# Kernel tuning notes

Measured on AMD Instinct MI355X. Metric: run time of the kernel, lower is better.

The kernel has to match this reference:

```python
import jax, jax.numpy as jnp
import numpy as np

N = 100000
E = 3200000
F_IN = 128
HID = 64
NUM_GRAPHS = 512
NUM_CLASSES = 2


def setup_inputs() -> dict:
    key = jax.random.key(0)
    ks = jax.random.split(key, 8)
    x = jax.random.normal(ks[0], (N, F_IN), dtype=jnp.float32)
    edge_index = jax.random.randint(ks[1], (2, E), 0, N, dtype=jnp.int64)
    batch = jnp.sort(jax.random.randint(ks[2], (N,), 0, NUM_GRAPHS, dtype=jnp.int64))
    # Glorot-style init for GCN weights, PyTorch default-style for fc
    W1 = jax.random.normal(ks[3], (F_IN, HID), dtype=jnp.float32) * (1.0 / np.sqrt(F_IN))
    b1 = jnp.zeros((HID,), dtype=jnp.float32)
    W2 = jax.random.normal(ks[4], (HID, HID), dtype=jnp.float32) * (1.0 / np.sqrt(HID))
    b2 = jnp.zeros((HID,), dtype=jnp.float32)
    Wfc = jax.random.normal(ks[5], (HID, NUM_CLASSES), dtype=jnp.float32) * (1.0 / np.sqrt(HID))
    bfc = jax.random.normal(ks[6], (NUM_CLASSES,), dtype=jnp.float32) * 0.01
    return {"x": x, "edge_index": edge_index, "batch": batch,
            "W1": W1, "b1": b1, "W2": W2, "b2": b2, "Wfc": Wfc, "bfc": bfc}


def _gcn_conv(x, row, col, deg_inv_sqrt, W, b):
    """PyG GCNConv: out[col] += d^{-1/2}[row] d^{-1/2}[col] * (x W)[row], self-loops included in row/col."""
    h = x @ W  # [N, out_dim]
    norm = deg_inv_sqrt[row] * deg_inv_sqrt[col]  # [E+N]
    msgs = h[row] * norm[:, None]  # gather + scale
    out = jax.ops.segment_sum(msgs, col, num_segments=N)  # scatter-add
    return out + b


def reference(x, edge_index, batch, W1, b1, W2, b2, Wfc, bfc):
    # add self-loops once (shared normalization for both layers)
    loop = jnp.arange(N, dtype=edge_index.dtype)
    row = jnp.concatenate([edge_index[0], loop])  # sources
    col = jnp.concatenate([edge_index[1], loop])  # targets
    deg = jax.ops.segment_sum(jnp.ones_like(col, dtype=x.dtype), col, num_segments=N)
    deg_inv_sqrt = jnp.where(deg > 0, jax.lax.rsqrt(deg), 0.0)

    h = jax.nn.relu(_gcn_conv(x, row, col, deg_inv_sqrt, W1, b1))
    h = jax.nn.relu(_gcn_conv(h, row, col, deg_inv_sqrt, W2, b2))

    # global_mean_pool over batch ids
    sums = jax.ops.segment_sum(h, batch, num_segments=NUM_GRAPHS)  # [G, HID]
    counts = jax.ops.segment_sum(jnp.ones((N,), dtype=h.dtype), batch, num_segments=NUM_GRAPHS)
    pooled = sums / jnp.maximum(counts, 1.0)[:, None]

    # dropout p=0.5 is identity in eval mode
    return pooled @ Wfc + bfc  # [G, NUM_CLASSES]
```

## Files before the change

kernel.cpp:

```cpp
#include <hip/hip_runtime.h>

#define N_NODES   100000
#define N_EDGES   3200000
#define F_INP     128
#define HID       64
#define N_GRAPHS  512
#define N_CLASSES 2
#define NB        782
#define SCAT_BLOCKS 1024
#define CHUNK     (N_EDGES / SCAT_BLOCKS)

__device__ __forceinline__ unsigned short f2bf(float f) {
    unsigned int u = __float_as_uint(f);
    return (unsigned short)((u + 0x7FFFu + ((u >> 16) & 1u)) >> 16);
}
__device__ __forceinline__ float bf_lo(unsigned int u) { return __uint_as_float(u << 16); }
__device__ __forceinline__ float bf_hi(unsigned int u) { return __uint_as_float(u & 0xFFFF0000u); }

__global__ __launch_bounds__(256) void hist_kernel(const int* __restrict__ ei,
                                                   int* __restrict__ bcnt,
                                                   int* __restrict__ bh) {
    __shared__ int hist[NB];
    for (int i = threadIdx.x; i < NB; i += 256) hist[i] = 0;
    __syncthreads();
    const int e0 = blockIdx.x * CHUNK, e1 = e0 + CHUNK;
    for (int e = e0 + threadIdx.x; e < e1; e += 256)
        atomicAdd(&hist[ei[N_EDGES + e] >> 7], 1);
    __syncthreads();
    for (int i = threadIdx.x; i < NB; i += 256) {
        int v = hist[i];
        bh[(size_t)blockIdx.x * NB + i] = v;
        if (v) atomicAdd(&bcnt[i], v);
    }
}

__global__ __launch_bounds__(1024) void scan_kernel(const int* __restrict__ bcnt,
                                                    int* __restrict__ boff) {
    __shared__ int s[1024];
    const int tid = threadIdx.x;
    const int v = (tid < NB) ? bcnt[tid] : 0;
    s[tid] = v;
    __syncthreads();
    for (int d = 1; d < 1024; d <<= 1) {
        int t = (tid >= d) ? s[tid - d] : 0;
        __syncthreads();
        s[tid] += t;
        __syncthreads();
    }
    if (tid <= NB) boff[tid] = s[tid] - v;
}

__global__ __launch_bounds__(64) void bbase_kernel(int* __restrict__ bh,
                                                   const int* __restrict__ boff) {
    const int b = blockIdx.x * 64 + threadIdx.x;
    if (b >= NB) return;
    int base = boff[b];
    for (int i = 0; i < SCAT_BLOCKS; i += 8) {
        int v[8];
#pragma unroll
        for (int j = 0; j < 8; ++j) v[j] = bh[(size_t)(i + j) * NB + b];
#pragma unroll
        for (int j = 0; j < 8; ++j) { bh[(size_t)(i + j) * NB + b] = base; base += v[j]; }
    }
}

__global__ __launch_bounds__(256) void scatter_kernel(const int* __restrict__ ei,
                                                      const int* __restrict__ bh,
                                                      int* __restrict__ pairs) {
    __shared__ int lbase[NB];
    __shared__ int lcur[NB];
    for (int i = threadIdx.x; i < NB; i += 256) {
        lbase[i] = bh[(size_t)blockIdx.x * NB + i];
        lcur[i] = 0;
    }
    __syncthreads();
    const int e0 = blockIdx.x * CHUNK, e1 = e0 + CHUNK;
    for (int e = e0 + threadIdx.x; e < e1; e += 256) {
        int c = ei[N_EDGES + e];
        int r = ei[e];
        int b = c >> 7;
        int off = atomicAdd(&lcur[b], 1);
        pairs[lbase[b] + off] = r | ((c & 127) << 17);
    }
}

__global__ __launch_bounds__(256) void csr_kernel(const int* __restrict__ pairs,
                                                  const int* __restrict__ boff,
                                                  int* __restrict__ adj,
                                                  int* __restrict__ offs,
                                                  float* __restrict__ dis) {
    __shared__ int cnt[128];
    __shared__ int sc[128];
    __shared__ int base[128];
    __shared__ int cur[128];
    const int tid = threadIdx.x;
    const int b = blockIdx.x;
    const int beg = boff[b], end = boff[b + 1];
    if (tid < 128) { cnt[tid] = 0; cur[tid] = 0; }
    __syncthreads();
    for (int e = beg + tid; e < end; e += 256)
        atomicAdd(&cnt[pairs[e] >> 17], 1);
    __syncthreads();
    if (tid < 128) sc[tid] = cnt[tid];
    __syncthreads();
    for (int d = 1; d < 128; d <<= 1) {
        int t = (tid >= d && tid < 128) ? sc[tid - d] : 0;
        __syncthreads();
        if (tid < 128) sc[tid] += t;
        __syncthreads();
    }
    if (tid < 128) base[tid] = beg + sc[tid] - cnt[tid];
    __syncthreads();
    for (int e = beg + tid; e < end; e += 256) {
        int v = pairs[e];
        int lc = v >> 17;
        int o = atomicAdd(&cur[lc], 1);
        adj[base[lc] + o] = v & 131071;
    }
    const int n = (b << 7) + tid;
    if (tid < 128 && n < N_NODES) {
        offs[n] = base[tid];
        dis[n] = rsqrtf((float)cnt[tid] + 1.0f);
    }
    if (b == 0 && tid == 0) offs[N_NODES] = N_EDGES;
}

#define MM1_ROWS 32
#define XS_LD    132
__global__ __launch_bounds__(256) void mm1_kernel(const float* __restrict__ x,
                                                  const float* __restrict__ W1,
                                                  const float* __restrict__ dis,
                                                  unsigned short* __restrict__ p) {
    __shared__ float xs[MM1_ROWS * XS_LD];
    __shared__ float ws[F_INP * HID];
    for (int i = threadIdx.x; i < F_INP * HID / 4; i += 256)
        ((float4*)ws)[i] = ((const float4*)W1)[i];
    const int row_base = blockIdx.x * MM1_ROWS;
    for (int i = threadIdx.x; i < MM1_ROWS * (F_INP / 4); i += 256) {
        int r = i >> 5, c4 = i & 31;
        int gr = row_base + r;
        float4 v = make_float4(0.f, 0.f, 0.f, 0.f);
        if (gr < N_NODES) v = *(const float4*)(x + (size_t)gr * F_INP + c4 * 4);
        *(float4*)(xs + r * XS_LD + c4 * 4) = v;
    }
    __syncthreads();
    const int tx = threadIdx.x & 15;
    const int ty = threadIdx.x >> 4;
    float acc[2][4] = {};
#pragma unroll 4
    for (int k = 0; k < F_INP; k += 4) {
        float4 a0 = *(const float4*)(xs + ty * XS_LD + k);
        float4 a1 = *(const float4*)(xs + (ty + 16) * XS_LD + k);
        float4 w0 = *(const float4*)(ws + (k + 0) * HID + tx * 4);
        float4 w1 = *(const float4*)(ws + (k + 1) * HID + tx * 4);
        float4 w2 = *(const float4*)(ws + (k + 2) * HID + tx * 4);
        float4 w3 = *(const float4*)(ws + (k + 3) * HID + tx * 4);
        acc[0][0] += a0.x * w0.x + a0.y * w1.x + a0.z * w2.x + a0.w * w3.x;
        acc[0][1] += a0.x * w0.y + a0.y * w1.y + a0.z * w2.y + a0.w * w3.y;
        acc[0][2] += a0.x * w0.z + a0.y * w1.z + a0.z * w2.z + a0.w * w3.z;
        acc[0][3] += a0.x * w0.w + a0.y * w1.w + a0.z * w2.w + a0.w * w3.w;
        acc[1][0] += a1.x * w0.x + a1.y * w1.x + a1.z * w2.x + a1.w * w3.x;
        acc[1][1] += a1.x * w0.y + a1.y * w1.y + a1.z * w2.y + a1.w * w3.y;
        acc[1][2] += a1.x * w0.z + a1.y * w1.z + a1.z * w2.z + a1.w * w3.z;
        acc[1][3] += a1.x * w0.w + a1.y * w1.w + a1.z * w2.w + a1.w * w3.w;
    }
#pragma unroll
    for (int i = 0; i < 2; ++i) {
        int rr = row_base + ty + 16 * i;
        if (rr < N_NODES) {
            float d = dis[rr];
            ushort4 o;
            o.x = f2bf(d * acc[i][0]);
            o.y = f2bf(d * acc[i][1]);
            o.z = f2bf(d * acc[i][2]);
            o.w = f2bf(d * acc[i][3]);
            *(ushort4*)(p + (size_t)rr * HID + tx * 4) = o;
        }
    }
}

#define HS_LD 72
__global__ __launch_bounds__(256) void mm2_kernel(const unsigned short* __restrict__ hb,
                                                  const float* __restrict__ W2,
                                                  const float* __restrict__ dis,
                                                  unsigned short* __restrict__ p) {
    __shared__ unsigned short hs[64 * HS_LD];
    __shared__ float ws[HID * HID];
    for (int i = threadIdx.x; i < HID * HID / 4; i += 256)
        ((float4*)ws)[i] = ((const float4*)W2)[i];
    const int row_base = blockIdx.x * 64;
    for (int i = threadIdx.x; i < 64 * (HID / 8); i += 256) {
        int r = i >> 3, c8 = i & 7;
        int gr = row_base + r;
        uint4 v = make_uint4(0u, 0u, 0u, 0u);
        if (gr < N_NODES) v = *(const uint4*)(hb + (size_t)gr * HID + c8 * 8);
        *(uint4*)(hs + r * HS_LD + c8 * 8) = v;
    }
    __syncthreads();
    const int tx = threadIdx.x & 15;
    const int ty = threadIdx.x >> 4;
    float acc[4][4] = {};
#pragma unroll 2
    for (int k = 0; k < HID; k += 8) {
        uint4 a[4];
#pragma unroll
        for (int i = 0; i < 4; ++i)
            a[i] = *(const uint4*)(hs + (ty + 16 * i) * HS_LD + k);
        float4 w[8];
#pragma unroll
        for (int m = 0; m < 8; ++m)
            w[m] = *(const float4*)(ws + (k + m) * HID + tx * 4);
#pragma unroll
        for (int i = 0; i < 4; ++i) {
            float h0 = bf_lo(a[i].x), h1 = bf_hi(a[i].x);
            float h2 = bf_lo(a[i].y), h3 = bf_hi(a[i].y);
            float h4 = bf_lo(a[i].z), h5 = bf_hi(a[i].z);
            float h6 = bf_lo(a[i].w), h7 = bf_hi(a[i].w);
            acc[i][0] += h0 * w[0].x + h1 * w[1].x + h2 * w[2].x + h3 * w[3].x
                       + h4 * w[4].x + h5 * w[5].x + h6 * w[6].x + h7 * w[7].x;
            acc[i][1] += h0 * w[0].y + h1 * w[1].y + h2 * w[2].y + h3 * w[3].y
                       + h4 * w[4].y + h5 * w[5].y + h6 * w[6].y + h7 * w[7].y;
            acc[i][2] += h0 * w[0].z + h1 * w[1].z + h2 * w[2].z + h3 * w[3].z
                       + h4 * w[4].z + h5 * w[5].z + h6 * w[6].z + h7 * w[7].z;
            acc[i][3] += h0 * w[0].w + h1 * w[1].w + h2 * w[2].w + h3 * w[3].w
                       + h4 * w[4].w + h5 * w[5].w + h6 * w[6].w + h7 * w[7].w;
        }
    }
#pragma unroll
    for (int i = 0; i < 4; ++i) {
        int rr = row_base + ty + 16 * i;
        if (rr < N_NODES) {
            float d = dis[rr];
            ushort4 o;
            o.x = f2bf(d * acc[i][0]);
            o.y = f2bf(d * acc[i][1]);
            o.z = f2bf(d * acc[i][2]);
            o.w = f2bf(d * acc[i][3]);
            *(ushort4*)(p + (size_t)rr * HID + tx * 4) = o;
        }
    }
}

__device__ __forceinline__ float gather_node(const unsigned short* __restrict__ p,
                                             const int* __restrict__ adj,
                                             int c, int beg, int end, int q, int g) {
    float acc[8];
    {
        uint4 s = *(const uint4*)(p + (size_t)c * HID + g * 8);
        float sm = (q == 0) ? 1.f : 0.f;
        acc[0] = sm * bf_lo(s.x); acc[1] = sm * bf_hi(s.x);
        acc[2] = sm * bf_lo(s.y); acc[3] = sm * bf_hi(s.y);
        acc[4] = sm * bf_lo(s.z); acc[5] = sm * bf_hi(s.z);
        acc[6] = sm * bf_lo(s.w); acc[7] = sm * bf_hi(s.w);
    }
    int e = beg;
    for (; e + 32 <= end; e += 32) {
        int r0 = adj[e + q];
        int r1 = adj[e + 8 + q];
        int r2 = adj[e + 16 + q];
        int r3 = adj[e + 24 + q];
        uint4 v0 = *(const uint4*)(p + (size_t)r0 * HID + g * 8);
        uint4 v1 = *(const uint4*)(p + (size_t)r1 * HID + g * 8);
        uint4 v2 = *(const uint4*)(p + (size_t)r2 * HID + g * 8);
        uint4 v3 = *(const uint4*)(p + (size_t)r3 * HID + g * 8);
        acc[0] += (bf_lo(v0.x) + bf_lo(v1.x)) + (bf_lo(v2.x) + bf_lo(v3.x));
        acc[1] += (bf_hi(v0.x) + bf_hi(v1.x)) + (bf_hi(v2.x) + bf_hi(v3.x));
        acc[2] += (bf_lo(v0.y) + bf_lo(v1.y)) + (bf_lo(v2.y) + bf_lo(v3.y));
        acc[3] += (bf_hi(v0.y) + bf_hi(v1.y)) + (bf_hi(v2.y) + bf_hi(v3.y));
        acc[4] += (bf_lo(v0.z) + bf_lo(v1.z)) + (bf_lo(v2.z) + bf_lo(v3.z));
        acc[5] += (bf_hi(v0.z) + bf_hi(v1.z)) + (bf_hi(v2.z) + bf_hi(v3.z));
        acc[6] += (bf_lo(v0.w) + bf_lo(v1.w)) + (bf_lo(v2.w) + bf_lo(v3.w));
        acc[7] += (bf_hi(v0.w) + bf_hi(v1.w)) + (bf_hi(v2.w) + bf_hi(v3.w));
    }
    for (; e + 16 <= end; e += 16) {
        int r0 = adj[e + q];
        int r1 = adj[e + 8 + q];
        uint4 v0 = *(const uint4*)(p + (size_t)r0 * HID + g * 8);
        uint4 v1 = *(const uint4*)(p + (size_t)r1 * HID + g * 8);
        acc[0] += bf_lo(v0.x) + bf_lo(v1.x); acc[1] += bf_hi(v0.x) + bf_hi(v1.x);
        acc[2] += bf_lo(v0.y) + bf_lo(v1.y); acc[3] += bf_hi(v0.y) + bf_hi(v1.y);
        acc[4] += bf_lo(v0.z) + bf_lo(v1.z); acc[5] += bf_hi(v0.z) + bf_hi(v1.z);
        acc[6] += bf_lo(v0.w) + bf_lo(v1.w); acc[7] += bf_hi(v0.w) + bf_hi(v1.w);
    }
    for (; e < end; e += 8) {
        int idx = e + q;
        int r = adj[min(idx, end - 1)];
        float m = (idx < end) ? 1.f : 0.f;
        uint4 v = *(const uint4*)(p + (size_t)r * HID + g * 8);
        acc[0] = fmaf(m, bf_lo(v.x), acc[0]); acc[1] = fmaf(m, bf_hi(v.x), acc[1]);
        acc[2] = fmaf(m, bf_lo(v.y), acc[2]); acc[3] = fmaf(m, bf_hi(v.y), acc[3]);
        acc[4] = fmaf(m, bf_lo(v.z), acc[4]); acc[5] = fmaf(m, bf_hi(v.z), acc[5]);
        acc[6] = fmaf(m, bf_lo(v.w), acc[6]); acc[7] = fmaf(m, bf_hi(v.w), acc[7]);
    }
    const bool q0 = (q & 1) != 0, q1 = (q & 2) != 0, q2 = (q & 4) != 0;
    float b0 = (q0 ? acc[1] : acc[0]) + __shfl_xor(q0 ? acc[0] : acc[1], 8, 64);
    float b1 = (q0 ? acc[3] : acc[2]) + __shfl_xor(q0 ? acc[2] : acc[3], 8, 64);
    float b2 = (q0 ? acc[5] : acc[4]) + __shfl_xor(q0 ? acc[4] : acc[5], 8, 64);
    float b3 = (q0 ? acc[7] : acc[6]) + __shfl_xor(q0 ? acc[6] : acc[7], 8, 64);
    float c0 = (q1 ? b1 : b0) + __shfl_xor(q1 ? b0 : b1, 16, 64);
    float c1 = (q1 ? b3 : b2) + __shfl_xor(q1 ? b2 : b3, 16, 64);
    return (q2 ? c1 : c0) + __shfl_xor(q2 ? c0 : c1, 32, 64);
}

__global__ __launch_bounds__(256) void gather1_kernel(const unsigned short* __restrict__ p,
                                                      const int* __restrict__ adj,
                                                      const int* __restrict__ offs,
                                                      const float* __restrict__ dis,
                                                      const float* __restrict__ b1,
                                                      unsigned short* __restrict__ hb) {
    const int lane = threadIdx.x & 63;
    const int q = lane >> 3, g = lane & 7;
    const int gwave = (blockIdx.x * blockDim.x + threadIdx.x) >> 6;
    const int nwaves = (gridDim.x * blockDim.x) >> 6;
    const int per = (N_NODES + nwaves - 1) / nwaves;
    const int c0 = gwave * per;
    const int c1 = min(N_NODES, c0 + per);
    const float bj = b1[g * 8 + q];
    if (c0 >= c1) return;
    int beg = offs[c0];
    for (int c = c0; c < c1; ++c) {
        const int end = offs[c + 1];
        float val = gather_node(p, adj, c, beg, end, q, g);
        hb[(size_t)c * HID + g * 8 + q] = f2bf(fmaxf(dis[c] * val + bj, 0.f));
        beg = end;
    }
}

__global__ __launch_bounds__(256) void gather2_kernel(const unsigned short* __restrict__ p,
                                                      const int* __restrict__ adj,
                                                      const int* __restrict__ offs,
                                                      const float* __restrict__ dis,
                                                      const float* __restrict__ b2,
                                                      const int* __restrict__ batch,
                                                      float* __restrict__ sums) {
    const int lane = threadIdx.x & 63;
    const int q = lane >> 3, g = lane & 7;
    const int gwave = (blockIdx.x * blockDim.x + threadIdx.x) >> 6;
    const int nwaves = (gridDim.x * blockDim.x) >> 6;
    const int per = (N_NODES + nwaves - 1) / nwaves;
    const int c0 = gwave * per;
    const int c1 = min(N_NODES, c0 + per);
    const float bj = b2[g * 8 + q];
    const int feat = g * 8 + q;
    float part = 0.f;
    int gc = -1;
    if (c0 >= c1) return;
    int beg = offs[c0];
    for (int c = c0; c < c1; ++c) {
        const int end = offs[c + 1];
        float val = gather_node(p, adj, c, beg, end, q, g);
        float v = fmaxf(dis[c] * val + bj, 0.f);
        int gid = batch[c];
        if (gid != gc) {
            if (gc >= 0) atomicAdd(&sums[(size_t)gc * HID + feat], part);
            part = 0.f;
            gc = gid;
        }
        part += v;
        beg = end;
    }
    if (gc >= 0) atomicAdd(&sums[(size_t)gc * HID + feat], part);
}

__global__ void fc_kernel(const float* __restrict__ sums, const int* __restrict__ batch,
                          const float* __restrict__ Wfc, const float* __restrict__ bfc,
                          float* __restrict__ out) {
    const int g = blockIdx.x;
    const int j = threadIdx.x;
    int lo = 0, hi = N_NODES;
    while (lo < hi) { int m = (lo + hi) >> 1; if (batch[m] < g) lo = m + 1; else hi = m; }
    const int l0 = lo;
    lo = 0; hi = N_NODES;
    while (lo < hi) { int m = (lo + hi) >> 1; if (batch[m] < g + 1) lo = m + 1; else hi = m; }
    float cnt = fmaxf((float)(lo - l0), 1.0f);
    float pj = sums[(size_t)g * HID + j] / cnt;
    float a0 = pj * Wfc[j * N_CLASSES + 0];
    float a1 = pj * Wfc[j * N_CLASSES + 1];
    for (int off = 32; off > 0; off >>= 1) {
        a0 += __shfl_down(a0, off, 64);
        a1 += __shfl_down(a1, off, 64);
    }
    if (j == 0) {
        out[g * N_CLASSES + 0] = a0 + bfc[0];
        out[g * N_CLASSES + 1] = a1 + bfc[1];
    }
}

extern "C" void kernel_launch(void* const* d_in, const int* in_sizes, int n_in,
                              void* d_out, int out_size, void* d_ws, size_t ws_size,
                              hipStream_t stream) {
    const float* x     = (const float*)d_in[0];
    const int*   ei    = (const int*)d_in[1];
    const int*   batch = (const int*)d_in[2];
    const float* W1    = (const float*)d_in[3];
    const float* b1    = (const float*)d_in[4];
    const float* W2    = (const float*)d_in[5];
    const float* b2    = (const float*)d_in[6];
    const float* Wfc   = (const float*)d_in[7];
    const float* bfc   = (const float*)d_in[8];
    float* out = (float*)d_out;

    char* ws = (char*)d_ws;
    size_t off = 0;
    auto alloc = [&](size_t bytes) -> void* {
        void* pp = ws + off;
        off += (bytes + 255) & ~(size_t)255;
        return pp;
    };
    int*   bcnt   = (int*)alloc((size_t)NB * 4);
    int*   boff   = (int*)alloc((size_t)(NB + 1) * 4);
    int*   bh     = (int*)alloc((size_t)SCAT_BLOCKS * NB * 4);
    float* dis    = (float*)alloc((size_t)N_NODES * 4);
    int*   pairs  = (int*)alloc((size_t)N_EDGES * 4);
    int*   adj    = (int*)alloc((size_t)N_EDGES * 4);
    int*   offs   = (int*)alloc((size_t)(N_NODES + 1) * 4);
    unsigned short* p  = (unsigned short*)alloc((size_t)N_NODES * HID * 2);
    unsigned short* hb = (unsigned short*)alloc((size_t)N_NODES * HID * 2);
    float* sums   = (float*)alloc((size_t)N_GRAPHS * HID * 4);

    hipMemsetAsync(bcnt, 0, (size_t)NB * 4, stream);
    hipMemsetAsync(sums, 0, (size_t)N_GRAPHS * HID * 4, stream);

    hist_kernel<<<SCAT_BLOCKS, 256, 0, stream>>>(ei, bcnt, bh);
    scan_kernel<<<1, 1024, 0, stream>>>(bcnt, boff);
    bbase_kernel<<<(NB + 63) / 64, 64, 0, stream>>>(bh, boff);
    scatter_kernel<<<SCAT_BLOCKS, 256, 0, stream>>>(ei, bh, pairs);
    csr_kernel<<<NB, 256, 0, stream>>>(pairs, boff, adj, offs, dis);
    mm1_kernel<<<(N_NODES + MM1_ROWS - 1) / MM1_ROWS, 256, 0, stream>>>(x, W1, dis, p);
    gather1_kernel<<<2048, 256, 0, stream>>>(p, adj, offs, dis, b1, hb);
    mm2_kernel<<<(N_NODES + 63) / 64, 256, 0, stream>>>(hb, W2, dis, p);
    gather2_kernel<<<2048, 256, 0, stream>>>(p, adj, offs, dis, b2, batch, sums);
    fc_kernel<<<N_GRAPHS, 64, 0, stream>>>(sums, batch, Wfc, bfc, out);
}
```

Baseline: 394.1 us.

## Build CSR with global degree atomics and direct placement instead of bucket sort

Replaces the two-level bucketed counting sort (per-block histograms, bucket scan, scatter to pairs, per-bucket local CSR) with a direct CSR build. It counts per-node degrees with global atomics, runs a three-kernel prefix scan, and places each edge with a global atomicAdd on a per-node cursor. This removes the intermediate pairs buffer, the large per-block histogram array and its strided rebasing pass. The cost is 3.2M contended global atomics in each of two passes, and adjacency order within a node becomes nondeterministic, which may hurt locality in the later gathers.

```diff
diff --git a/kernel.cpp b/kernel.cpp
--- a/kernel.cpp
+++ b/kernel.cpp
@@ -6,9 +6,8 @@
 #define HID       64
 #define N_GRAPHS  512
 #define N_CLASSES 2
-#define NB        782
-#define SCAT_BLOCKS 1024
-#define CHUNK     (N_EDGES / SCAT_BLOCKS)
+#define SCAN_BLKS 98
+#define EDGE_BLKS 2048
 
 __device__ __forceinline__ unsigned short f2bf(float f) {
     unsigned int u = __float_as_uint(f);
@@ -17,28 +16,21 @@
 __device__ __forceinline__ float bf_lo(unsigned int u) { return __uint_as_float(u << 16); }
 __device__ __forceinline__ float bf_hi(unsigned int u) { return __uint_as_float(u & 0xFFFF0000u); }
 
-__global__ __launch_bounds__(256) void hist_kernel(const int* __restrict__ ei,
-                                                   int* __restrict__ bcnt,
-                                                   int* __restrict__ bh) {
-    __shared__ int hist[NB];
-    for (int i = threadIdx.x; i < NB; i += 256) hist[i] = 0;
-    __syncthreads();
-    const int e0 = blockIdx.x * CHUNK, e1 = e0 + CHUNK;
-    for (int e = e0 + threadIdx.x; e < e1; e += 256)
-        atomicAdd(&hist[ei[N_EDGES + e] >> 7], 1);
-    __syncthreads();
-    for (int i = threadIdx.x; i < NB; i += 256) {
-        int v = hist[i];
-        bh[(size_t)blockIdx.x * NB + i] = v;
-        if (v) atomicAdd(&bcnt[i], v);
-    }
-}
-
-__global__ __launch_bounds__(1024) void scan_kernel(const int* __restrict__ bcnt,
-                                                    int* __restrict__ boff) {
+__global__ __launch_bounds__(256) void deg_kernel(const int* __restrict__ ei,
+                                                  int* __restrict__ cnt) {
+    int e = blockIdx.x * 256 + threadIdx.x;
+    const int st = EDGE_BLKS * 256;
+    for (; e < N_EDGES; e += st)
+        atomicAdd(&cnt[ei[N_EDGES + e]], 1);
+}
+
+__global__ __launch_bounds__(1024) void s1_kernel(const int* __restrict__ cnt,
+                                                  int* __restrict__ part,
+                                                  int* __restrict__ bsum) {
     __shared__ int s[1024];
     const int tid = threadIdx.x;
-    const int v = (tid < NB) ? bcnt[tid] : 0;
+    const int gid = blockIdx.x * 1024 + tid;
+    const int v = (gid < N_NODES) ? cnt[gid] : 0;
     s[tid] = v;
     __syncthreads();
     for (int d = 1; d < 1024; d <<= 1) {
@@ -47,82 +39,52 @@
         s[tid] += t;
         __syncthreads();
     }
-    if (tid <= NB) boff[tid] = s[tid] - v;
-}
-
-__global__ __launch_bounds__(64) void bbase_kernel(int* __restrict__ bh,
-                                                   const int* __restrict__ boff) {
-    const int b = blockIdx.x * 64 + threadIdx.x;
-    if (b >= NB) return;
-    int base = boff[b];
-    for (int i = 0; i < SCAT_BLOCKS; i += 8) {
-        int v[8];
-#pragma unroll
-        for (int j = 0; j < 8; ++j) v[j] = bh[(size_t)(i + j) * NB + b];
-#pragma unroll
-        for (int j = 0; j < 8; ++j) { bh[(size_t)(i + j) * NB + b] = base; base += v[j]; }
-    }
-}
-
-__global__ __launch_bounds__(256) void scatter_kernel(const int* __restrict__ ei,
-                                                      const int* __restrict__ bh,
-                                                      int* __restrict__ pairs) {
-    __shared__ int lbase[NB];
-    __shared__ int lcur[NB];
-    for (int i = threadIdx.x; i < NB; i += 256) {
-        lbase[i] = bh[(size_t)blockIdx.x * NB + i];
-        lcur[i] = 0;
-    }
-    __syncthreads();
-    const int e0 = blockIdx.x * CHUNK, e1 = e0 + CHUNK;
-    for (int e = e0 + threadIdx.x; e < e1; e += 256) {
-        int c = ei[N_EDGES + e];
-        int r = ei[e];
-        int b = c >> 7;
-        int off = atomicAdd(&lcur[b], 1);
-        pairs[lbase[b] + off] = r | ((c & 127) << 17);
-    }
-}
-
-__global__ __launch_bounds__(256) void csr_kernel(const int* __restrict__ pairs,
-                                                  const int* __restrict__ boff,
-                                                  int* __restrict__ adj,
-                                                  int* __restrict__ offs,
-                                                  float* __restrict__ dis) {
-    __shared__ int cnt[128];
-    __shared__ int sc[128];
-    __shared__ int base[128];
-    __shared__ int cur[128];
+    if (gid < N_NODES) part[gid] = s[tid] - v;
+    if (tid == 1023) bsum[blockIdx.x] = s[1023];
+}
+
+__global__ __launch_bounds__(128) void s2_kernel(int* __restrict__ bsum) {
+    __shared__ int s[128];
     const int tid = threadIdx.x;
-    const int b = blockIdx.x;
-    const int beg = boff[b], end = boff[b + 1];
-    if (tid < 128) { cnt[tid] = 0; cur[tid] = 0; }
-    __syncthreads();
-    for (int e = beg + tid; e < end; e += 256)
-        atomicAdd(&cnt[pairs[e] >> 17], 1);
-    __syncthreads();
-    if (tid < 128) sc[tid] = cnt[tid];
+    const int v = (tid < SCAN_BLKS) ? bsum[tid] : 0;
+    s[tid] = v;
     __syncthreads();
     for (int d = 1; d < 128; d <<= 1) {
-        int t = (tid >= d && tid < 128) ? sc[tid - d] : 0;
+        int t = (tid >= d) ? s[tid - d] : 0;
         __syncthreads();
-        if (tid < 128) sc[tid] += t;
+        s[tid] += t;
         __syncthreads();
     }
-    if (tid < 128) base[tid] = beg + sc[tid] - cnt[tid];
-    __syncthreads();
-    for (int e = beg + tid; e < end; e += 256) {
-        int v = pairs[e];
-        int lc = v >> 17;
-        int o = atomicAdd(&cur[lc], 1);
-        adj[base[lc] + o] = v & 131071;
-    }
-    const int n = (b << 7) + tid;
-    if (tid < 128 && n < N_NODES) {
-        offs[n] = base[tid];
-        dis[n] = rsqrtf((float)cnt[tid] + 1.0f);
-    }
-    if (b == 0 && tid == 0) offs[N_NODES] = N_EDGES;
+    if (tid < SCAN_BLKS) bsum[tid] = s[tid] - v;
+}
+
+__global__ __launch_bounds__(1024) void s3_kernel(const int* __restrict__ cnt,
+                                                  const int* __restrict__ part,
+                                                  const int* __restrict__ bsum,
+                                                  int* __restrict__ offs,
+                                                  int* __restrict__ cur,
+                                                  float* __restrict__ dis) {
+    const int gid = blockIdx.x * 1024 + threadIdx.x;
+    if (gid < N_NODES) {
+        const int o = part[gid] + bsum[blockIdx.x];
+        offs[gid] = o;
+        cur[gid] = o;
+        dis[gid] = rsqrtf((float)cnt[gid] + 1.0f);
+    }
+    if (gid == 0) offs[N_NODES] = N_EDGES;
+}
+
+__global__ __launch_bounds__(256) void place_kernel(const int* __restrict__ ei,
+                                                    int* __restrict__ cur,
+                                                    int* __restrict__ adj) {
+    int e = blockIdx.x * 256 + threadIdx.x;
+    const int st = EDGE_BLKS * 256;
+    for (; e < N_EDGES; e += st) {
+        const int c = ei[N_EDGES + e];
+        const int r = ei[e];
+        const int pos = atomicAdd(&cur[c], 1);
+        adj[pos] = r;
+    }
 }
 
 #define MM1_ROWS 32
@@ -407,25 +369,25 @@
         off += (bytes + 255) & ~(size_t)255;
         return pp;
     };
-    int*   bcnt   = (int*)alloc((size_t)NB * 4);
-    int*   boff   = (int*)alloc((size_t)(NB + 1) * 4);
-    int*   bh     = (int*)alloc((size_t)SCAT_BLOCKS * NB * 4);
+    int*   cnt    = (int*)alloc((size_t)N_NODES * 4);
+    int*   part   = (int*)alloc((size_t)N_NODES * 4);
+    int*   bsum   = (int*)alloc((size_t)128 * 4);
+    int*   offs   = (int*)alloc((size_t)(N_NODES + 1) * 4);
+    int*   cur    = (int*)alloc((size_t)N_NODES * 4);
     float* dis    = (float*)alloc((size_t)N_NODES * 4);
-    int*   pairs  = (int*)alloc((size_t)N_EDGES * 4);
     int*   adj    = (int*)alloc((size_t)N_EDGES * 4);
-    int*   offs   = (int*)alloc((size_t)(N_NODES + 1) * 4);
     unsigned short* p  = (unsigned short*)alloc((size_t)N_NODES * HID * 2);
     unsigned short* hb = (unsigned short*)alloc((size_t)N_NODES * HID * 2);
     float* sums   = (float*)alloc((size_t)N_GRAPHS * HID * 4);
 
-    hipMemsetAsync(bcnt, 0, (size_t)NB * 4, stream);
+    hipMemsetAsync(cnt, 0, (size_t)N_NODES * 4, stream);
     hipMemsetAsync(sums, 0, (size_t)N_GRAPHS * HID * 4, stream);
 
-    hist_kernel<<<SCAT_BLOCKS, 256, 0, stream>>>(ei, bcnt, bh);
-    scan_kernel<<<1, 1024, 0, stream>>>(bcnt, boff);
-    bbase_kernel<<<(NB + 63) / 64, 64, 0, stream>>>(bh, boff);
-    scatter_kernel<<<SCAT_BLOCKS, 256, 0, stream>>>(ei, bh, pairs);
-    csr_kernel<<<NB, 256, 0, stream>>>(pairs, boff, adj, offs, dis);
+    deg_kernel<<<EDGE_BLKS, 256, 0, stream>>>(ei, cnt);
+    s1_kernel<<<SCAN_BLKS, 1024, 0, stream>>>(cnt, part, bsum);
+    s2_kernel<<<1, 128, 0, stream>>>(bsum);
+    s3_kernel<<<SCAN_BLKS, 1024, 0, stream>>>(cnt, part, bsum, offs, cur, dis);
+    place_kernel<<<EDGE_BLKS, 256, 0, stream>>>(ei, cur, adj);
     mm1_kernel<<<(N_NODES + MM1_ROWS - 1) / MM1_ROWS, 256, 0, stream>>>(x, W1, dis, p);
     gather1_kernel<<<2048, 256, 0, stream>>>(p, adj, offs, dis, b1, hb);
     mm2_kernel<<<(N_NODES + 63) / 64, 256, 0, stream>>>(hb, W2, dis, p);
```

Result: slower. 685.1 us (+73.8%).
